# Optimization experiments

Hardware: AMD Instinct MI355X
Metric: run time of the kernel (lower is better)

The kernel has to match this reference:

```python
import jax, jax.numpy as jnp
import numpy as np

B, S, H = 4, 1024, 1024
NHEADS = 16
DK = H // NHEADS


def setup_inputs() -> dict:
    key = jax.random.key(0)
    ks = jax.random.split(key, 9)
    scale = 1.0 / np.sqrt(H).astype(np.float32)
    query = jax.random.normal(ks[0], (B, S, H), dtype=jnp.float32)
    key_in = jax.random.normal(ks[1], (B, S, H), dtype=jnp.float32)
    score_mask = jax.random.randint(ks[2], (B, S, S), 0, 2).astype(bool)
    # torch nn.Linear params, stored as [in, out] so y = x @ W + b
    Wq = jax.random.normal(ks[3], (H, H), dtype=jnp.float32) * scale
    bq = jax.random.normal(ks[4], (H,), dtype=jnp.float32) * scale
    Wk = jax.random.normal(ks[5], (H, H), dtype=jnp.float32) * scale
    bk = jax.random.normal(ks[6], (H,), dtype=jnp.float32) * scale
    Wp = jax.random.normal(ks[7], (H, H), dtype=jnp.float32) * scale
    bp = jax.random.normal(ks[8], (H,), dtype=jnp.float32) * scale
    return dict(query=query, key_in=key_in, score_mask=score_mask,
                Wq=Wq, bq=bq, Wk=Wk, bk=bk, Wp=Wp, bp=bp)


def reference(query, key_in, score_mask, Wq, bq, Wk, bk, Wp, bp):
    # Projections + head split: [B,S,H] -> [B,h,S,dk]
    q = (query @ Wq + bq).reshape(B, S, NHEADS, DK).transpose(0, 2, 1, 3)
    k = (key_in @ Wk + bk).reshape(B, S, NHEADS, DK).transpose(0, 2, 1, 3)
    inv_sqrt_dk = jnp.asarray(1.0 / np.sqrt(DK), dtype=q.dtype)
    scores = jnp.einsum('bhqd,bhkd->bhqk', q, k) * inv_sqrt_dk
    # masked_fill(score_mask.unsqueeze(1), -1e9): mask True = masked, broadcast over heads
    scores = jnp.where(score_mask[:, None, :, :], jnp.asarray(-1e9, scores.dtype), scores)
    # redundant per-row mask multiply: b = ~mask[:, None, :, 0:1]
    row_keep = (~score_mask[:, None, :, 0:1]).astype(scores.dtype)  # [B,1,S,1]
    p_attn = jax.nn.softmax(scores, axis=-1) * row_keep
    # NON-STANDARD: value is the projected query, not a separate value tensor
    out = jnp.einsum('bhqk,bhkd->bhqd', p_attn, q)
    out = out.transpose(0, 2, 1, 3).reshape(B, S, H)  # merge heads
    return out @ Wp + bp
```

## Files before the change

kernel.cpp:

```cpp
#include <hip/hip_runtime.h>
#include <hip/hip_bf16.h>

using bf16x8 = __attribute__((ext_vector_type(8))) short;
using f32x4  = __attribute__((ext_vector_type(4))) float;

static __device__ __forceinline__ short f2bf(float f) {
  union { float f; unsigned u; } x; x.f = f;
  unsigned r = x.u + 0x7fffu + ((x.u >> 16) & 1u);
  return (short)(r >> 16);
}
static __device__ __forceinline__ float bf2f(short b) {
  union { unsigned u; float f; } x; x.u = ((unsigned)(unsigned short)b) << 16;
  return x.f;
}
static __device__ __forceinline__ unsigned pack_bf2(float lo, float hi) {
  __hip_bfloat162 h = __float22bfloat162_rn(float2{lo, hi});
  unsigned u; __builtin_memcpy(&u, &h, 4); return u;
}
static __device__ __forceinline__ float exp2_raw(float x) {
  float r; asm("v_exp_f32 %0, %1" : "=v"(r) : "v"(x)); return r;
}
static __device__ __forceinline__ void gll16(const void* g, void* l) {
  __builtin_amdgcn_global_load_lds((__attribute__((address_space(1))) const void*)g,
                                   (__attribute__((address_space(3))) void*)l, 16, 0, 0);
}

__global__ void k_pack_mask(const unsigned* __restrict__ src_u32,
                            unsigned long long* __restrict__ out, int n) {
  unsigned probe = src_u32[threadIdx.x & 63];
  const bool u8mode = (__ballot(probe > 1u) != 0ull);
  const unsigned char* s8 = (const unsigned char*)src_u32;
  const int* s32 = (const int*)src_u32;
  for (int e = blockIdx.x * blockDim.x + threadIdx.x; e < n; e += gridDim.x * blockDim.x) {
    int v = u8mode ? (int)s8[e] : s32[e];
    unsigned long long b = __ballot(v != 0);
    if ((threadIdx.x & 63) == 0) out[e >> 6] = b;
  }
}

__global__ void k_cvt_bf16(const float* __restrict__ in0, short* __restrict__ out0,
                           const float* __restrict__ in1, short* __restrict__ out1, int n4) {
  const float* in = blockIdx.y ? in1 : in0;
  short* out = blockIdx.y ? out1 : out0;
  for (int i = blockIdx.x * blockDim.x + threadIdx.x; i < n4; i += gridDim.x * blockDim.x) {
    float4 v = reinterpret_cast<const float4*>(in)[i];
    short4 o;
    o.x = f2bf(v.x); o.y = f2bf(v.y); o.z = f2bf(v.z); o.w = f2bf(v.w);
    reinterpret_cast<short4*>(out)[i] = o;
  }
}

__global__ void k_transpose_cvt(const float* __restrict__ W0, const float* __restrict__ W1,
                                const float* __restrict__ W2, short* __restrict__ out3) {
  __shared__ float tile[32][33];
  const float* in = blockIdx.z == 0 ? W0 : (blockIdx.z == 1 ? W1 : W2);
  short* out = out3 + (size_t)blockIdx.z * 1024 * 1024;
  int x = blockIdx.x * 32 + threadIdx.x;
  int y0 = blockIdx.y * 32;
  for (int j = 0; j < 32; j += 8)
    tile[threadIdx.y + j][threadIdx.x] = in[(size_t)(y0 + threadIdx.y + j) * 1024 + x];
  __syncthreads();
  int xo = blockIdx.y * 32 + threadIdx.x;
  int yo = blockIdx.x * 32;
  for (int j = 0; j < 32; j += 8)
    out[(size_t)(yo + threadIdx.y + j) * 1024 + xo] = f2bf(tile[threadIdx.x][threadIdx.y + j]);
}

__global__ void k_vt_transpose(const short* __restrict__ Qp, short* __restrict__ Vtg) {
  __shared__ short T[64 * 64];
  const int st = blockIdx.x, h = blockIdx.y, b = blockIdx.z;
  const int tid = threadIdx.x;
#pragma unroll
  for (int c = 0; c < 2; ++c) {
    int ch = c * 256 + tid;
    int row = ch >> 3, cn = ch & 7;
    bf16x8 v = *reinterpret_cast<const bf16x8*>(
        &Qp[(size_t)(b * 1024 + st * 64 + row) * 1024 + h * 64 + cn * 8]);
    *reinterpret_cast<bf16x8*>(&T[row * 64 + ((cn ^ (row & 7)) * 8)]) = v;
  }
  __syncthreads();
#pragma unroll
  for (int c = 0; c < 2; ++c) {
    int ch = c * 256 + tid;
    int d = ch >> 3, sc = ch & 7;
    bf16x8 v;
#pragma unroll
    for (int j = 0; j < 8; ++j) {
      int s_loc = sc * 8 + j;
      v[j] = T[s_loc * 64 + (((d >> 3) ^ j) * 8) + (d & 7)];
    }
    *reinterpret_cast<bf16x8*>(
        &Vtg[(size_t)((b * 16 + h) * 64 + d) * 1024 + st * 64 + sc * 8]) = v;
  }
}

template<int OUT_BF16, int BN, int M, int N, int K>
__device__ __forceinline__ void gemm_body(const short* __restrict__ A,
                                          const short* __restrict__ Bt,
                                          const float* __restrict__ bias,
                                          void* __restrict__ C) {
  __shared__ short Al[2][128 * 64];
  __shared__ short Bl[2][BN * 64];
  constexpr int JF = BN / 32;
  const int tid  = threadIdx.x;
  const int lane = tid & 63, wid = tid >> 6;
  const int g = lane >> 4, lr = lane & 15;
  const int wm = wid >> 1, wn = wid & 1;
  constexpr int nbx = N / BN;
  constexpr int nwg = nbx * (M >> 7);
  const int lin = blockIdx.y * nbx + blockIdx.x;
  const int orig = (lin & 7) * (nwg >> 3) + (lin >> 3);
  const int m0 = (orig / nbx) * 128, n0 = (orig % nbx) * BN;
  const int srow = lane >> 3;
  const int sch  = ((lane & 7) ^ srow) * 8;

  f32x4 acc[4][JF];
#pragma unroll
  for (int i = 0; i < 4; ++i)
#pragma unroll
    for (int j = 0; j < JF; ++j) acc[i][j] = (f32x4){0.f, 0.f, 0.f, 0.f};

  constexpr int NT = K >> 6;
  auto stage = [&](int buf, int kt) {
#pragma unroll
    for (int s = 0; s < 4; ++s)
      gll16(&A[(size_t)(m0 + s * 32 + wid * 8 + srow) * K + kt + sch],
            &Al[buf][(s * 32 + wid * 8) * 64]);
#pragma unroll
    for (int s = 0; s < BN / 32; ++s)
      gll16(&Bt[(size_t)(n0 + s * 32 + wid * 8 + srow) * K + kt + sch],
            &Bl[buf][(s * 32 + wid * 8) * 64]);
  };

  stage(0, 0);
  asm volatile("s_waitcnt vmcnt(0)" ::: "memory");
  __builtin_amdgcn_s_barrier();
  asm volatile("" ::: "memory");

#pragma unroll 1
  for (int t = 0; t < NT; ++t) {
    const int cur = t & 1;
    if (t + 1 < NT) stage(cur ^ 1, (t + 1) * 64);
#pragma unroll
    for (int kb = 0; kb < 2; ++kb) {
      const int cs = ((kb * 4 + g) ^ (lr & 7)) * 8;
      bf16x8 af[4], bfr[JF];
#pragma unroll
      for (int i = 0; i < 4; ++i)
        af[i] = *reinterpret_cast<const bf16x8*>(&Al[cur][(wm * 64 + i * 16 + lr) * 64 + cs]);
#pragma unroll
      for (int j = 0; j < JF; ++j)
        bfr[j] = *reinterpret_cast<const bf16x8*>(
            &Bl[cur][(wn * (BN / 2) + j * 16 + lr) * 64 + cs]);
#pragma unroll
      for (int i = 0; i < 4; ++i)
#pragma unroll
        for (int j = 0; j < JF; ++j)
          acc[i][j] = __builtin_amdgcn_mfma_f32_16x16x32_bf16(af[i], bfr[j], acc[i][j], 0, 0, 0);
    }
    if (t + 1 < NT) {
      asm volatile("s_waitcnt vmcnt(0)" ::: "memory");
      __builtin_amdgcn_s_barrier();
      asm volatile("" ::: "memory");
    }
  }

#pragma unroll
  for (int i = 0; i < 4; ++i) {
    int row = m0 + wm * 64 + i * 16 + g * 4;
#pragma unroll
    for (int j = 0; j < JF; ++j) {
      int col = n0 + wn * (BN / 2) + j * 16 + lr;
      float bv = bias[col];
#pragma unroll
      for (int r = 0; r < 4; ++r) {
        float v = acc[i][j][r] + bv;
        if (OUT_BF16) ((short*)C)[(size_t)(row + r) * N + col] = f2bf(v);
        else          ((float*)C)[(size_t)(row + r) * N + col] = v;
      }
    }
  }
}

__launch_bounds__(256)
__global__ void k_gemm_qk(const short* __restrict__ A0, const short* __restrict__ A1,
                          const short* __restrict__ Bt3,
                          const float* __restrict__ b0, const float* __restrict__ b1,
                          short* __restrict__ C0, short* __restrict__ C1) {
  if (blockIdx.z == 0) gemm_body<1, 128, 4096, 1024, 1024>(A0, Bt3,               b0, C0);
  else                 gemm_body<1, 128, 4096, 1024, 1024>(A1, Bt3 + 1024 * 1024, b1, C1);
}

__launch_bounds__(256)
__global__ void k_gemm_out(const short* __restrict__ A, const short* __restrict__ Bt,
                           const float* __restrict__ bias, float* __restrict__ C) {
  gemm_body<0, 64, 4096, 1024, 1024>(A, Bt, bias, C);
}

__launch_bounds__(512)
__global__ void k_attention(const short* __restrict__ Qp, const short* __restrict__ Kp,
                            const short* __restrict__ Vtg,
                            const unsigned long long* __restrict__ mb,
                            short* __restrict__ O) {
  __shared__ short Kl[3][64 * 64];
  __shared__ short Vl[3][64 * 64];
  __shared__ short Pl[8][16 * 64];
  const int tid  = threadIdx.x;
  const int lane = tid & 63, wid = tid >> 6;
  const int g = lane >> 4, lr = lane & 15;
  const int g4 = 4 * g;
  const int bid = (blockIdx.x & 7) * 64 + (blockIdx.x >> 3);
  const int qt = bid & 7, h = (bid >> 3) & 15, b = bid >> 7;
  const int qb = qt * 128 + wid * 16;
  const int srow = lane >> 3;
  const int sch  = ((lane & 7) ^ srow) * 8;

  const size_t qrow = (size_t)(b * 1024 + qb + lr);
  const float qs = 0.125f * 1.44269504088896340736f;
  bf16x8 aq[2];
#pragma unroll
  for (int db = 0; db < 2; ++db) {
    bf16x8 raw = *reinterpret_cast<const bf16x8*>(&Qp[qrow * 1024 + h * 64 + db * 32 + g * 8]);
#pragma unroll
    for (int j = 0; j < 8; j += 2) {
      unsigned pk = pack_bf2(bf2f(raw[j]) * qs, bf2f(raw[j + 1]) * qs);
      aq[db][j]     = (short)(pk & 0xffffu);
      aq[db][j + 1] = (short)(pk >> 16);
    }
  }

  const unsigned long long* mrow = &mb[qrow * 16];
  const short* Ksrc = &Kp[(size_t)(b * 1024 + wid * 8 + srow) * 1024 + h * 64 + sch];
  const short* Vsrc = &Vtg[(size_t)((b * 16 + h) * 64 + wid * 8 + srow) * 1024 + sch];

  f32x4 o[4];
#pragma unroll
  for (int d = 0; d < 4; ++d) o[d] = (f32x4){0.f, 0.f, 0.f, 0.f};
  float l_part = 0.f;
  short* Prow = &Pl[wid][lr * 64];

  gll16(Ksrc,                     &Kl[0][(wid * 8) * 64]);
  gll16(Vsrc,                     &Vl[0][(wid * 8) * 64]);
  gll16(Ksrc + (size_t)64 * 1024, &Kl[1][(wid * 8) * 64]);
  gll16(Vsrc + 64,                &Vl[1][(wid * 8) * 64]);
  unsigned long long mwA = mrow[0];
  unsigned long long mwB = mrow[1];
  unsigned long long mwC = 0;
  const float keep = (mwA & 1ull) ? 0.f : 1.f;

  int cur = 0;
  int b2  = 2;
#pragma unroll 1
  for (int kt = 0; kt < 16; ++kt) {
    if (kt >= 1) {
      const short* Vb = Vl[b2];
      __builtin_amdgcn_s_setprio(1);
#pragma unroll
      for (int kb = 0; kb < 2; ++kb) {
        bf16x8 pa = *reinterpret_cast<const bf16x8*>(
            &Prow[(((kb * 4 + g) ^ (lr & 7)) * 8)]);
        const int cs = ((kb * 4 + g) ^ (lr & 7)) * 8;
#pragma unroll
        for (int d = 0; d < 4; ++d) {
          bf16x8 vf = *reinterpret_cast<const bf16x8*>(&Vb[(d * 16 + lr) * 64 + cs]);
          o[d] = __builtin_amdgcn_mfma_f32_16x16x32_bf16(vf, pa, o[d], 0, 0, 0);
        }
      }
      __builtin_amdgcn_s_setprio(0);
    }

    if (kt < 15) asm volatile("s_waitcnt vmcnt(4)" ::: "memory");
    else         asm volatile("s_waitcnt vmcnt(0)" ::: "memory");
    __builtin_amdgcn_s_barrier();
    asm volatile("" ::: "memory");

    if (kt + 2 < 16) {
      gll16(Ksrc + (size_t)(kt + 2) * 64 * 1024, &Kl[b2][(wid * 8) * 64]);
      gll16(Vsrc + (kt + 2) * 64,                &Vl[b2][(wid * 8) * 64]);
      mwC = mrow[kt + 2];
    }

    const unsigned mlo = (unsigned)mwA;
    const unsigned mhi = (unsigned)(mwA >> 32);

#pragma unroll
    for (int kc = 0; kc < 4; ++kc) {
      f32x4 a = (f32x4){0.f, 0.f, 0.f, 0.f};
      __builtin_amdgcn_s_setprio(1);
#pragma unroll
      for (int db = 0; db < 2; ++db) {
        bf16x8 kf = *reinterpret_cast<const bf16x8*>(
            &Kl[cur][(kc * 16 + lr) * 64 + (((db * 4 + g) ^ (lr & 7)) * 8)]);
        a = __builtin_amdgcn_mfma_f32_16x16x32_bf16(kf, aq[db], a, 0, 0, 0);
      }
      __builtin_amdgcn_s_setprio(0);
      const unsigned wk = ((kc < 2 ? mlo : mhi) >> (((kc & 1) << 4) + g4)) & 0xFu;
      float p0 = (wk & 1u) ? 0.f : exp2_raw(a[0]);
      float p1 = (wk & 2u) ? 0.f : exp2_raw(a[1]);
      float p2 = (wk & 4u) ? 0.f : exp2_raw(a[2]);
      float p3 = (wk & 8u) ? 0.f : exp2_raw(a[3]);
      l_part += (p0 + p1) + (p2 + p3);
      unsigned lo = pack_bf2(p0, p1), hi = pack_bf2(p2, p3);
      unsigned long long w = (unsigned long long)lo | ((unsigned long long)hi << 32);
      *reinterpret_cast<unsigned long long*>(
          &Prow[((2 * kc + (g >> 1)) ^ (lr & 7)) * 8 + (g & 1) * 4]) = w;
    }
    mwA = mwB; mwB = mwC;
    cur = (cur == 2) ? 0 : cur + 1;
    b2  = (b2  == 2) ? 0 : b2  + 1;
    asm volatile("" ::: "memory");
  }

  {
    const short* Vb = Vl[0];
    __builtin_amdgcn_s_setprio(1);
#pragma unroll
    for (int kb = 0; kb < 2; ++kb) {
      bf16x8 pa = *reinterpret_cast<const bf16x8*>(
          &Prow[(((kb * 4 + g) ^ (lr & 7)) * 8)]);
      const int cs = ((kb * 4 + g) ^ (lr & 7)) * 8;
#pragma unroll
      for (int d = 0; d < 4; ++d) {
        bf16x8 vf = *reinterpret_cast<const bf16x8*>(&Vb[(d * 16 + lr) * 64 + cs]);
        o[d] = __builtin_amdgcn_mfma_f32_16x16x32_bf16(vf, pa, o[d], 0, 0, 0);
      }
    }
    __builtin_amdgcn_s_setprio(0);
  }

  float l_run = l_part;
  l_run += __shfl_xor(l_run, 16);
  l_run += __shfl_xor(l_run, 32);

  const float inv = (l_run > 0.f) ? keep / l_run : 0.f;
#pragma unroll
  for (int d = 0; d < 4; ++d) {
    unsigned lo = pack_bf2(o[d][0] * inv, o[d][1] * inv);
    unsigned hi = pack_bf2(o[d][2] * inv, o[d][3] * inv);
    unsigned long long w = (unsigned long long)lo | ((unsigned long long)hi << 32);
    *reinterpret_cast<unsigned long long*>(
        &Prow[((2 * d + (g >> 1)) ^ (lr & 7)) * 8 + (g & 1) * 4]) = w;
  }
#pragma unroll
  for (int it = 0; it < 2; ++it) {
    int qq = it * 8 + srow;
    bf16x8 val = *reinterpret_cast<const bf16x8*>(
        &Pl[wid][qq * 64 + (((lane & 7) ^ (qq & 7)) * 8)]);
    *reinterpret_cast<bf16x8*>(
        &O[(size_t)(b * 1024 + qt * 128 + wid * 16 + qq) * 1024 + h * 64 + (lane & 7) * 8]) = val;
  }
}

extern "C" void kernel_launch(void* const* d_in, const int* in_sizes, int n_in,
                              void* d_out, int out_size, void* d_ws, size_t ws_size,
                              hipStream_t stream) {
  const float* query  = (const float*)d_in[0];
  const float* key_in = (const float*)d_in[1];
  const void*  mask_raw = d_in[2];
  const float* Wq = (const float*)d_in[3];
  const float* bq = (const float*)d_in[4];
  const float* Wk = (const float*)d_in[5];
  const float* bk = (const float*)d_in[6];
  const float* Wp = (const float*)d_in[7];
  const float* bp = (const float*)d_in[8];

  char* ws = (char*)d_ws;
  size_t off = 0;
  auto alloc = [&](size_t bytes) {
    char* p = ws + off;
    off = (off + bytes + 255) & ~(size_t)255;
    return p;
  };
  unsigned long long* packb = (unsigned long long*)alloc(512ull << 10);
  short* Qbf   = (short*)alloc(8ull << 20);
  short* Kbf   = (short*)alloc(8ull << 20);
  short* Wt3   = (short*)alloc(6ull << 20);
  short* Qproj = (short*)alloc(8ull << 20);
  short* Kproj = (short*)alloc(8ull << 20);
  short* Vtg   = (short*)alloc(8ull << 20);
  short* AttnO = Kbf;

  k_pack_mask<<<2048, 256, 0, stream>>>((const unsigned*)mask_raw, packb, 4 * 1024 * 1024);
  k_cvt_bf16<<<dim3(1024, 2), 256, 0, stream>>>(query, Qbf, key_in, Kbf,
                                                (4 * 1024 * 1024) / 4);
  k_transpose_cvt<<<dim3(32, 32, 3), dim3(32, 8), 0, stream>>>(Wq, Wk, Wp, Wt3);

  dim3 gqk(8, 32, 2);
  k_gemm_qk<<<gqk, 256, 0, stream>>>(Qbf, Kbf, Wt3, bq, bk, Qproj, Kproj);

  k_vt_transpose<<<dim3(16, 16, 4), 256, 0, stream>>>(Qproj, Vtg);
  k_attention<<<512, 512, 0, stream>>>(Qproj, Kproj, Vtg, packb, AttnO);

  k_gemm_out<<<dim3(16, 32), 256, 0, stream>>>(AttnO, Wt3 + 2 * 1024 * 1024, bp,
                                               (float*)d_out);
}
```

Measured before the change: 105.1 us.

## Merge prep kernels into one launch and fuse V-transpose into Q-projection GEMM epilogue

Three preprocessing kernels (mask bit-packing, fp32→bf16 activation conversion, weight transpose-convert) are merged into one block-indexed launch. The separate V-transpose kernel is removed: the Q-projection GEMM epilogue writes the transposed, biased bf16 tile through LDS straight into the Vtg layout. This cuts two kernel launches and one full read of Qproj from global memory. In exchange the Q-GEMM blocks do extra LDS and store work, and that half of the GEMM becomes slower than the K half.

Result: slower. 111.6 us (+6.2%).

```diff
diff --git a/kernel.cpp b/kernel.cpp
--- a/kernel.cpp
+++ b/kernel.cpp
@@ -25,80 +25,60 @@
                                    (__attribute__((address_space(3))) void*)l, 16, 0, 0);
 }
 
-__global__ void k_pack_mask(const unsigned* __restrict__ src_u32,
-                            unsigned long long* __restrict__ out, int n) {
-  unsigned probe = src_u32[threadIdx.x & 63];
-  const bool u8mode = (__ballot(probe > 1u) != 0ull);
-  const unsigned char* s8 = (const unsigned char*)src_u32;
-  const int* s32 = (const int*)src_u32;
-  for (int e = blockIdx.x * blockDim.x + threadIdx.x; e < n; e += gridDim.x * blockDim.x) {
-    int v = u8mode ? (int)s8[e] : s32[e];
-    unsigned long long b = __ballot(v != 0);
-    if ((threadIdx.x & 63) == 0) out[e >> 6] = b;
-  }
-}
-
-__global__ void k_cvt_bf16(const float* __restrict__ in0, short* __restrict__ out0,
-                           const float* __restrict__ in1, short* __restrict__ out1, int n4) {
-  const float* in = blockIdx.y ? in1 : in0;
-  short* out = blockIdx.y ? out1 : out0;
-  for (int i = blockIdx.x * blockDim.x + threadIdx.x; i < n4; i += gridDim.x * blockDim.x) {
-    float4 v = reinterpret_cast<const float4*>(in)[i];
-    short4 o;
-    o.x = f2bf(v.x); o.y = f2bf(v.y); o.z = f2bf(v.z); o.w = f2bf(v.w);
-    reinterpret_cast<short4*>(out)[i] = o;
-  }
-}
-
-__global__ void k_transpose_cvt(const float* __restrict__ W0, const float* __restrict__ W1,
-                                const float* __restrict__ W2, short* __restrict__ out3) {
-  __shared__ float tile[32][33];
-  const float* in = blockIdx.z == 0 ? W0 : (blockIdx.z == 1 ? W1 : W2);
-  short* out = out3 + (size_t)blockIdx.z * 1024 * 1024;
-  int x = blockIdx.x * 32 + threadIdx.x;
-  int y0 = blockIdx.y * 32;
-  for (int j = 0; j < 32; j += 8)
-    tile[threadIdx.y + j][threadIdx.x] = in[(size_t)(y0 + threadIdx.y + j) * 1024 + x];
-  __syncthreads();
-  int xo = blockIdx.y * 32 + threadIdx.x;
-  int yo = blockIdx.x * 32;
-  for (int j = 0; j < 32; j += 8)
-    out[(size_t)(yo + threadIdx.y + j) * 1024 + xo] = f2bf(tile[threadIdx.x][threadIdx.y + j]);
-}
-
-__global__ void k_vt_transpose(const short* __restrict__ Qp, short* __restrict__ Vtg) {
-  __shared__ short T[64 * 64];
-  const int st = blockIdx.x, h = blockIdx.y, b = blockIdx.z;
-  const int tid = threadIdx.x;
-#pragma unroll
-  for (int c = 0; c < 2; ++c) {
-    int ch = c * 256 + tid;
-    int row = ch >> 3, cn = ch & 7;
-    bf16x8 v = *reinterpret_cast<const bf16x8*>(
-        &Qp[(size_t)(b * 1024 + st * 64 + row) * 1024 + h * 64 + cn * 8]);
-    *reinterpret_cast<bf16x8*>(&T[row * 64 + ((cn ^ (row & 7)) * 8)]) = v;
-  }
-  __syncthreads();
-#pragma unroll
-  for (int c = 0; c < 2; ++c) {
-    int ch = c * 256 + tid;
-    int d = ch >> 3, sc = ch & 7;
-    bf16x8 v;
-#pragma unroll
-    for (int j = 0; j < 8; ++j) {
-      int s_loc = sc * 8 + j;
-      v[j] = T[s_loc * 64 + (((d >> 3) ^ j) * 8) + (d & 7)];
-    }
-    *reinterpret_cast<bf16x8*>(
-        &Vtg[(size_t)((b * 16 + h) * 64 + d) * 1024 + st * 64 + sc * 8]) = v;
-  }
-}
-
-template<int OUT_BF16, int BN, int M, int N, int K>
+__global__ void k_prep(const float* __restrict__ query, const float* __restrict__ key_in,
+                       const float* __restrict__ Wq, const float* __restrict__ Wk,
+                       const float* __restrict__ Wp,
+                       const unsigned* __restrict__ mask_u32,
+                       short* __restrict__ Qbf, short* __restrict__ Kbf,
+                       short* __restrict__ Wt3, unsigned long long* __restrict__ packb) {
+  const int bid = blockIdx.x, tid = threadIdx.x;
+  if (bid < 2048) {
+    const float* in = bid < 1024 ? query : key_in;
+    short* out = bid < 1024 ? Qbf : Kbf;
+    const int r = bid & 1023;
+    const int n4 = (4 * 1024 * 1024) / 4;
+    for (int i = r * 256 + tid; i < n4; i += 1024 * 256) {
+      float4 v = reinterpret_cast<const float4*>(in)[i];
+      short4 o;
+      o.x = f2bf(v.x); o.y = f2bf(v.y); o.z = f2bf(v.z); o.w = f2bf(v.w);
+      reinterpret_cast<short4*>(out)[i] = o;
+    }
+  } else if (bid < 5120) {
+    __shared__ float tile[32][33];
+    const int sub = bid - 2048;
+    const int w = sub >> 10, s2 = sub & 1023;
+    const int bx = s2 & 31, by = s2 >> 5;
+    const float* in = w == 0 ? Wq : (w == 1 ? Wk : Wp);
+    short* out = Wt3 + (size_t)w * 1024 * 1024;
+    const int tx = tid & 31, ty = tid >> 5;
+    int x = bx * 32 + tx, y0 = by * 32;
+    for (int j = 0; j < 32; j += 8)
+      tile[ty + j][tx] = in[(size_t)(y0 + ty + j) * 1024 + x];
+    __syncthreads();
+    int xo = by * 32 + tx, yo = bx * 32;
+    for (int j = 0; j < 32; j += 8)
+      out[(size_t)(yo + ty + j) * 1024 + xo] = f2bf(tile[tx][ty + j]);
+  } else {
+    const int r = bid - 5120;
+    unsigned probe = mask_u32[tid & 63];
+    const bool u8mode = (__ballot(probe > 1u) != 0ull);
+    const unsigned char* s8 = (const unsigned char*)mask_u32;
+    const int* s32 = (const int*)mask_u32;
+    const int n = 4 * 1024 * 1024;
+    for (int e = r * 256 + tid; e < n; e += 2048 * 256) {
+      int v = u8mode ? (int)s8[e] : s32[e];
+      unsigned long long b = __ballot(v != 0);
+      if ((tid & 63) == 0) packb[e >> 6] = b;
+    }
+  }
+}
+
+template<int OUT_BF16, int BN, int M, int N, int K, int VT_OUT>
 __device__ __forceinline__ void gemm_body(const short* __restrict__ A,
                                           const short* __restrict__ Bt,
                                           const float* __restrict__ bias,
-                                          void* __restrict__ C) {
+                                          void* __restrict__ C,
+                                          short* __restrict__ Vtg) {
   __shared__ short Al[2][128 * 64];
   __shared__ short Bl[2][BN * 64];
   constexpr int JF = BN / 32;
@@ -180,21 +160,57 @@
       }
     }
   }
+
+  if (VT_OUT) {
+    short* T = (short*)Al;
+    __builtin_amdgcn_s_barrier();
+    asm volatile("" ::: "memory");
+#pragma unroll
+    for (int i = 0; i < 4; ++i) {
+      int row = wm * 64 + i * 16 + g * 4;
+#pragma unroll
+      for (int j = 0; j < JF; ++j) {
+        int col = wn * (BN / 2) + j * 16 + lr;
+        float bv = bias[n0 + col];
+        unsigned d0 = pack_bf2(acc[i][j][0] + bv, acc[i][j][1] + bv);
+        unsigned d1 = pack_bf2(acc[i][j][2] + bv, acc[i][j][3] + bv);
+        unsigned long long w = (unsigned long long)d0 | ((unsigned long long)d1 << 32);
+        *reinterpret_cast<unsigned long long*>(
+            &T[col * 128 + (row ^ ((col & 7) << 4))]) = w;
+      }
+    }
+    __builtin_amdgcn_s_barrier();
+    asm volatile("" ::: "memory");
+    const int bb = m0 >> 10, s0 = m0 & 1023, h0 = n0 >> 6;
+#pragma unroll
+    for (int it = 0; it < 8; ++it) {
+      int ch = it * 256 + tid;
+      int d_loc = ch >> 4, sc = ch & 15;
+      bf16x8 v = *reinterpret_cast<const bf16x8*>(
+          &T[d_loc * 128 + ((sc * 8) ^ ((d_loc & 7) << 4))]);
+      *reinterpret_cast<bf16x8*>(
+          &Vtg[(size_t)((bb * 16 + h0 + (d_loc >> 6)) * 64 + (d_loc & 63)) * 1024
+               + s0 + sc * 8]) = v;
+    }
+  }
 }
 
 __launch_bounds__(256)
 __global__ void k_gemm_qk(const short* __restrict__ A0, const short* __restrict__ A1,
                           const short* __restrict__ Bt3,
                           const float* __restrict__ b0, const float* __restrict__ b1,
-                          short* __restrict__ C0, short* __restrict__ C1) {
-  if (blockIdx.z == 0) gemm_body<1, 128, 4096, 1024, 1024>(A0, Bt3,               b0, C0);
-  else                 gemm_body<1, 128, 4096, 1024, 1024>(A1, Bt3 + 1024 * 1024, b1, C1);
+                          short* __restrict__ C0, short* __restrict__ C1,
+                          short* __restrict__ Vtg) {
+  if (blockIdx.z == 0)
+    gemm_body<1, 128, 4096, 1024, 1024, 1>(A0, Bt3,               b0, C0, Vtg);
+  else
+    gemm_body<1, 128, 4096, 1024, 1024, 0>(A1, Bt3 + 1024 * 1024, b1, C1, nullptr);
 }
 
 __launch_bounds__(256)
 __global__ void k_gemm_out(const short* __restrict__ A, const short* __restrict__ Bt,
                            const float* __restrict__ bias, float* __restrict__ C) {
-  gemm_body<0, 64, 4096, 1024, 1024>(A, Bt, bias, C);
+  gemm_body<0, 64, 4096, 1024, 1024, 0>(A, Bt, bias, C, nullptr);
 }
 
 __launch_bounds__(512)
@@ -380,15 +396,12 @@
   short* Vtg   = (short*)alloc(8ull << 20);
   short* AttnO = Kbf;
 
-  k_pack_mask<<<2048, 256, 0, stream>>>((const unsigned*)mask_raw, packb, 4 * 1024 * 1024);
-  k_cvt_bf16<<<dim3(1024, 2), 256, 0, stream>>>(query, Qbf, key_in, Kbf,
-                                                (4 * 1024 * 1024) / 4);
-  k_transpose_cvt<<<dim3(32, 32, 3), dim3(32, 8), 0, stream>>>(Wq, Wk, Wp, Wt3);
+  k_prep<<<7168, 256, 0, stream>>>(query, key_in, Wq, Wk, Wp,
+                                   (const unsigned*)mask_raw, Qbf, Kbf, Wt3, packb);
 
   dim3 gqk(8, 32, 2);
-  k_gemm_qk<<<gqk, 256, 0, stream>>>(Qbf, Kbf, Wt3, bq, bk, Qproj, Kproj);
-
-  k_vt_transpose<<<dim3(16, 16, 4), 256, 0, stream>>>(Qproj, Vtg);
+  k_gemm_qk<<<gqk, 256, 0, stream>>>(Qbf, Kbf, Wt3, bq, bk, Qproj, Kproj, Vtg);
+
   k_attention<<<512, 512, 0, stream>>>(Qproj, Kproj, Vtg, packb, AttnO);
 
   k_gemm_out<<<dim3(16, 32), 256, 0, stream>>>(AttnO, Wt3 + 2 * 1024 * 1024, bp,
```
